# Optimization experiments

Hardware: AMD Instinct MI355X
Metric: run time of the kernel (lower is better)

## Reference

```python
import jax, jax.numpy as jnp
import numpy as np

N_NODES = 8192
N_EDGES = 131072
BATCH = 2
HID = 256      # hidden_dim
MSG = 256      # message_dim
EDIM = 64      # edge feature dim
MLP_H = 512    # message MLP hidden width
OUT = 128      # readout dim
N_ITERS = 3


def setup_inputs() -> dict:
    key = jax.random.key(0)
    ks = jax.random.split(key, 20)
    s = 0.05  # small init so iterated GRU stays well-conditioned
    inp = {
        "edge_feat": jax.random.normal(ks[0], (N_EDGES, BATCH, EDIM), jnp.float32),
        "W1": jax.random.normal(ks[1], (HID + HID + EDIM, MLP_H), jnp.float32) * s,
        "b1": jnp.zeros((MLP_H,), jnp.float32),
        "W2": jax.random.normal(ks[2], (MLP_H, MSG), jnp.float32) * s,
        "b2": jnp.zeros((MSG,), jnp.float32),
        "Wr": jax.random.normal(ks[3], (MSG, HID), jnp.float32) * s,
        "Ur": jax.random.normal(ks[4], (HID, HID), jnp.float32) * s,
        "br": jnp.zeros((HID,), jnp.float32),
        "Wz": jax.random.normal(ks[5], (MSG, HID), jnp.float32) * s,
        "Uz": jax.random.normal(ks[6], (HID, HID), jnp.float32) * s,
        "bz": jnp.zeros((HID,), jnp.float32),
        "Wh": jax.random.normal(ks[7], (MSG, HID), jnp.float32) * s,
        "Uh": jax.random.normal(ks[8], (HID, HID), jnp.float32) * s,
        "bh": jnp.zeros((HID,), jnp.float32),
        "Wo": jax.random.normal(ks[9], (HID, OUT), jnp.float32) * s,
        "bo": jnp.zeros((OUT,), jnp.float32),
        "edge_src": jax.random.randint(ks[10], (N_EDGES,), 0, N_NODES, jnp.int32),
        "edge_dst": jax.random.randint(ks[11], (N_EDGES,), 0, N_NODES, jnp.int32),
    }
    return inp


def reference(edge_feat, W1, b1, W2, b2, Wr, Ur, br, Wz, Uz, bz,
              Wh, Uh, bh, Wo, bo, edge_src, edge_dst):
    # reset_hidden_states: zeros for hidden and persistent message accumulator
    h = jnp.zeros((N_NODES, BATCH, HID), edge_feat.dtype)
    m = jnp.zeros((N_NODES, BATCH, MSG), edge_feat.dtype)

    for _ in range(N_ITERS):
        # gather endpoint hiddens: h_v = receiver (dst), h_w = sender (src)
        h_v = h[edge_dst]                       # [E, B, HID]
        h_w = h[edge_src]                       # [E, B, HID]
        x = jnp.concatenate([h_v, h_w, edge_feat], axis=-1)  # [E, B, 576]
        # per-edge message MLP
        msg = jax.nn.relu(x @ W1 + b1) @ W2 + b2              # [E, B, MSG]
        # scatter-sum into receiving nodes; accumulator persists across iters
        m = m + jax.ops.segment_sum(msg, edge_dst, num_segments=N_NODES)
        # GRU vertex update: h = GRU(m, h)
        r = jax.nn.sigmoid(m @ Wr + h @ Ur + br)
        z = jax.nn.sigmoid(m @ Wz + h @ Uz + bz)
        h_tilde = jnp.tanh(m @ Wh + (r * h) @ Uh + bh)
        h = (1.0 - z) * h + z * h_tilde

    # readout: sum node hiddens, then linear
    g = jnp.sum(h, axis=0)                      # [B, HID]
    return g @ Wo + bo                          # [B, OUT]
```

## Files before the change

kernel.cpp:

```cpp
#include <hip/hip_runtime.h>
#include <hip/hip_bf16.h>

#define E_EDGES 131072
#define NNODES  8192
#define NB      16384
#define HID     256
#define EDIM    64
#define MLPH    512
#define OUTD    128
#define NIT     3
#define RB      32

typedef short s16x4 __attribute__((ext_vector_type(4)));
typedef short s16x8 __attribute__((ext_vector_type(8)));
typedef float f32x4 __attribute__((ext_vector_type(4)));
typedef float f32x2 __attribute__((ext_vector_type(2)));

__device__ __forceinline__ short f2bf(float f){
  unsigned int x = __builtin_bit_cast(unsigned int, f);
  x += 0x7fffu + ((x >> 16) & 1u);
  return (short)(x >> 16);
}
__device__ __forceinline__ float bf2f(short s){
  unsigned int x = ((unsigned int)(unsigned short)s) << 16;
  return __builtin_bit_cast(float, x);
}
__device__ __forceinline__ void gload_lds16(const void* g, void* l){
  __builtin_amdgcn_global_load_lds(
      (const __attribute__((address_space(1))) void*)g,
      (__attribute__((address_space(3))) void*)l, 16, 0, 0);
}
#define MFMA16(a,b,c) __builtin_amdgcn_mfma_f32_16x16x32_bf16((a),(b),(c),0,0,0)

#if defined(__has_builtin)
#if __has_builtin(__builtin_amdgcn_cvt_pk_f32_fp8) && __has_builtin(__builtin_amdgcn_cvt_pk_fp8_f32)
#define FP8_HW 1
#endif
#endif
#ifndef FP8_HW
#define FP8_HW 0
#endif

__device__ __forceinline__ unsigned char enc_fp8_sw(float f){
  unsigned int b = __builtin_bit_cast(unsigned int, f);
  unsigned int s = (b >> 24) & 0x80u;
  float a = fabsf(f);
  if (a >= 448.f) return (unsigned char)(s | 0x7e);
  if (a < 0.015625f){
    int q = (int)rintf(a * 512.f);
    return (unsigned char)(s | (unsigned int)q);
  }
  unsigned int e32  = (b >> 23) & 0xff;
  unsigned int mant = b & 0x7fffff;
  unsigned int rnd  = mant + 0x7ffff + ((mant >> 20) & 1);
  unsigned int e8   = e32 - 120 + (rnd >> 23);
  unsigned int m3   = (rnd >> 20) & 7;
  if (e8 >= 16) return (unsigned char)(s | 0x7e);
  return (unsigned char)(s | (e8 << 3) | m3);
}
__device__ __forceinline__ float dec_fp8_sw(unsigned int v){
  unsigned int s = (v >> 7) & 1, e = (v >> 3) & 15, m = v & 7;
  float r;
  if (e == 0) r = (float)m * 0.001953125f;
  else        r = __builtin_bit_cast(float, ((e + 120u) << 23) | (m << 20));
  return s ? -r : r;
}
__device__ __forceinline__ unsigned char enc_fp8(float f){
#if FP8_HW
  unsigned int pk = (unsigned int)__builtin_amdgcn_cvt_pk_fp8_f32(f, f, 0, false);
  return (unsigned char)(pk & 0xff);
#else
  return enc_fp8_sw(f);
#endif
}
__device__ __forceinline__ void dec_fp8x4(unsigned int ev, float& e0, float& e1,
                                          float& e2, float& e3){
#if FP8_HW
  f32x2 lo = __builtin_amdgcn_cvt_pk_f32_fp8((int)ev, false);
  f32x2 hi = __builtin_amdgcn_cvt_pk_f32_fp8((int)ev, true);
  e0 = lo[0]; e1 = lo[1]; e2 = hi[0]; e3 = hi[1];
#else
  e0 = dec_fp8_sw(ev & 0xff); e1 = dec_fp8_sw((ev >> 8) & 0xff);
  e2 = dec_fp8_sw((ev >> 16) & 0xff); e3 = dec_fp8_sw(ev >> 24);
#endif
}

__global__ __launch_bounds__(256, 4)
void e1_gemm(const float* __restrict__ ef, const short* __restrict__ BtE,
             unsigned char* __restrict__ E1, const float* __restrict__ b1,
             const int* __restrict__ ceid)
{
  __shared__ __align__(16) short As[128 * 64];
  __shared__ __align__(16) short Bs[128 * 64];

  const int t  = threadIdx.x;
  const int w  = t >> 6, l = t & 63;
  const int lr = l & 15, lg = l >> 4;
  const int wr = w >> 1, wc = w & 1;
  const int browbase = blockIdx.x * 128;
  const int bcolbase = blockIdx.y * 128;
  const int srow = t >> 3;
  const int scol = (t & 7) * 8;

#pragma unroll
  for (int i = 0; i < 4; ++i)
    gload_lds16(BtE + (size_t)(bcolbase + srow + i * 32) * 64 + scol,
                (char*)Bs + w * 1024 + i * 4096);

#pragma unroll
  for (int i = 0; i < 4; ++i){
    int R = browbase + srow + i * 32;
    int e = ceid[R >> 1];
    const float* ap = ef + ((size_t)e * 2 + (R & 1)) * EDIM + scol;
    f32x4 f0 = *(const f32x4*)ap;
    f32x4 f1 = *(const f32x4*)(ap + 4);
    s16x8 o;
    o[0]=f2bf(f0[0]); o[1]=f2bf(f0[1]); o[2]=f2bf(f0[2]); o[3]=f2bf(f0[3]);
    o[4]=f2bf(f1[0]); o[5]=f2bf(f1[1]); o[6]=f2bf(f1[2]); o[7]=f2bf(f1[3]);
    int row = srow + i * 32;
    *(s16x8*)(As + row * 64 + (scol ^ ((row & 7) << 3))) = o;
  }
  __syncthreads();

  f32x4 acc[4][4];
#pragma unroll
  for (int mm = 0; mm < 4; ++mm)
#pragma unroll
    for (int n = 0; n < 4; ++n) acc[mm][n] = (f32x4){0.f,0.f,0.f,0.f};

#pragma unroll
  for (int kk = 0; kk < 2; ++kk){
    s16x8 a[4], b[4];
#pragma unroll
    for (int mm = 0; mm < 4; ++mm){
      int ar = wr*64 + mm*16 + lr;
      a[mm] = *(const s16x8*)(As + ar * 64 + ((kk*32 + lg*8) ^ ((ar & 7) << 3)));
    }
#pragma unroll
    for (int n = 0; n < 4; ++n){
      int br = wc*64 + n*16 + lr;
      b[n] = *(const s16x8*)(Bs + br * 64 + ((kk*32 + lg*8) ^ ((br & 7) << 3)));
    }
#pragma unroll
    for (int mm = 0; mm < 4; ++mm)
#pragma unroll
      for (int n = 0; n < 4; ++n)
        acc[mm][n] = MFMA16(a[mm], b[n], acc[mm][n]);
  }
#pragma unroll
  for (int mm = 0; mm < 4; ++mm){
    int orow0 = browbase + wr*64 + mm*16 + lg*4;
#pragma unroll
    for (int n = 0; n < 4; ++n){
      int ocol = bcolbase + wc*64 + n*16 + lr;
#pragma unroll
      for (int r = 0; r < 4; ++r)
        E1[(size_t)(orow0 + r) * MLPH + ocol] = enc_fp8(acc[mm][n][r] + b1[ocol]);
    }
  }
}

template<bool USE_P>
__global__ __launch_bounds__(256)
void edge_kernel(const short* __restrict__ P, const unsigned char* __restrict__ E1,
                 const int* __restrict__ csr_src, const int* __restrict__ row_start,
                 short* __restrict__ S)
{
  const int n = blockIdx.x;
  const int t = threadIdx.x;
  const int b = t >> 7;
  const int j = (t & 127) << 2;
  const int ps = row_start[n], pe = row_start[n + 1];

  float p10 = 0.f, p11 = 0.f, p12 = 0.f, p13 = 0.f;
  if (USE_P){
    s16x4 t1 = *(const s16x4*)(P + (size_t)(n * 2 + b) * 1024 + j);
    p10 = bf2f(t1[0]); p11 = bf2f(t1[1]); p12 = bf2f(t1[2]); p13 = bf2f(t1[3]);
  }
  float a0 = 0.f, a1 = 0.f, a2 = 0.f, a3 = 0.f;
  for (int p = ps; p < pe; ++p){
    unsigned int ev = *(const unsigned int*)(E1 + ((size_t)p * 2 + b) * 512 + j);
    float e0, e1, e2, e3;
    dec_fp8x4(ev, e0, e1, e2, e3);
    float x0 = p10 + e0, x1 = p11 + e1, x2 = p12 + e2, x3 = p13 + e3;
    if (USE_P){
      int src = csr_src[p];
      s16x4 v2 = *(const s16x4*)(P + (size_t)(src * 2 + b) * 1024 + 512 + j);
      x0 += bf2f(v2[0]); x1 += bf2f(v2[1]); x2 += bf2f(v2[2]); x3 += bf2f(v2[3]);
    }
    a0 += fmaxf(x0, 0.f); a1 += fmaxf(x1, 0.f);
    a2 += fmaxf(x2, 0.f); a3 += fmaxf(x3, 0.f);
  }
  s16x4 o; o[0] = f2bf(a0); o[1] = f2bf(a1); o[2] = f2bf(a2); o[3] = f2bf(a3);
  *(s16x4*)(S + (size_t)(n * 2 + b) * 512 + j) = o;
}

template<int PH>
__global__ __launch_bounds__(256, 2)
void node_update(const short* __restrict__ S, short* __restrict__ Pout,
                 float* __restrict__ m, float* __restrict__ h,
                 float* __restrict__ g,
                 const short* __restrict__ BtW2, const short* __restrict__ BtRZ,
                 const short* __restrict__ BtHW, const short* __restrict__ BtP,
                 const int* __restrict__ deg, const float* __restrict__ b2,
                 const float* __restrict__ br, const float* __restrict__ bz,
                 const float* __restrict__ bh)
{
  __shared__ __align__(16) char lds[69632];
  short* As = (short*)lds;
  short* Bs = (short*)(lds + 4096);
  short* Ms = (short*)(lds + 36864);
  short* Xs = (short*)(lds + 53248);
  float* Hf = (float*)lds;

  const int tid = threadIdx.x;
  const int w = tid >> 6, l = tid & 63;
  const int lr = l & 15, lg = l >> 4;
  const int grow0 = blockIdx.x * RB;

  auto stageB = [&](const short* Bt, int K, int pcol0, int k0){
#pragma unroll
    for (int i = 0; i < 8; ++i){
      int u = i * 256 + tid;
      int row = u >> 3, uc = u & 7;
      const short* gp = Bt + (size_t)(pcol0 + row) * K + k0 + ((uc ^ (row & 7)) << 3);
      gload_lds16(gp, (char*)Bs + i * 4096 + w * 1024);
    }
  };
  auto stageA_S = [&](int k0){
    int row = tid >> 3, uc = tid & 7;
    const short* gp = S + (size_t)(grow0 + row) * 512 + k0 + ((uc ^ (row & 7)) << 3);
    gload_lds16(gp, (char*)As + w * 1024);
  };
  auto rdA64 = [&](int row, int colel){ return row * 64 + (colel ^ ((row & 7) << 3)); };
  auto rd256 = [&](int row, int colel){ return row * 256 + (colel ^ ((row & 7) << 3)); };

  f32x4 hv[2][4], acc[2][4];
#pragma unroll
  for (int i = 0; i < 2; ++i)
#pragma unroll
    for (int j = 0; j < 4; ++j)
#pragma unroll
      for (int r = 0; r < 4; ++r){
        int rl = i*16 + lg*4 + r, colp = w*64 + j*16 + lr;
        size_t gi = (size_t)(grow0 + rl) * 256 + colp;
        float base = (float)deg[(grow0 + rl) >> 1] * b2[colp];
        if (PH > 0){ base += m[gi]; hv[i][j][r] = h[gi]; }
        else hv[i][j][r] = 0.f;
        acc[i][j][r] = base;
      }
  if (PH > 0){
#pragma unroll
    for (int i = 0; i < 2; ++i)
#pragma unroll
      for (int j = 0; j < 4; ++j)
#pragma unroll
        for (int r = 0; r < 4; ++r){
          int rl = i*16 + lg*4 + r, colp = w*64 + j*16 + lr;
          Xs[rd256(rl, colp)] = f2bf(hv[i][j][r]);
        }
  }

  for (int c = 0; c < 8; ++c){
    __syncthreads();
    stageA_S(c * 64);
    stageB(BtW2, 512, 0, c * 64);
    __syncthreads();
#pragma unroll
    for (int kk = 0; kk < 2; ++kk){
      s16x8 a0 = *(const s16x8*)(As + rdA64(lr,      kk*32 + lg*8));
      s16x8 a1 = *(const s16x8*)(As + rdA64(16 + lr, kk*32 + lg*8));
#pragma unroll
      for (int j = 0; j < 4; ++j){
        s16x8 bb = *(const s16x8*)(Bs + rdA64(w*64 + j*16 + lr, kk*32 + lg*8));
        acc[0][j] = MFMA16(a0, bb, acc[0][j]);
        acc[1][j] = MFMA16(a1, bb, acc[1][j]);
      }
    }
  }
#pragma unroll
  for (int i = 0; i < 2; ++i)
#pragma unroll
    for (int j = 0; j < 4; ++j)
#pragma unroll
      for (int r = 0; r < 4; ++r){
        int rl = i*16 + lg*4 + r, colp = w*64 + j*16 + lr;
        float v = acc[i][j][r];
        if (PH < 2) m[(size_t)(grow0 + rl) * 256 + colp] = v;
        Ms[rd256(rl, colp)] = f2bf(v);
      }

  const int NC = (PH > 0) ? 8 : 4;

  f32x4 Gr[2][4], Gz[2][4];
#pragma unroll
  for (int i = 0; i < 2; ++i)
#pragma unroll
    for (int j = 0; j < 4; ++j){ Gr[i][j] = (f32x4){0.f,0.f,0.f,0.f}; Gz[i][j] = (f32x4){0.f,0.f,0.f,0.f}; }

  for (int c = 0; c < NC; ++c){
    __syncthreads();
    stageB(BtRZ, 512, 0, c * 64);
    __syncthreads();
    const short* Ab = (c < 4) ? Ms : Xs;
    int kb = (c & 3) * 64;
#pragma unroll
    for (int kk = 0; kk < 2; ++kk){
      s16x8 a0 = *(const s16x8*)(Ab + rd256(lr,      kb + kk*32 + lg*8));
      s16x8 a1 = *(const s16x8*)(Ab + rd256(16 + lr, kb + kk*32 + lg*8));
#pragma unroll
      for (int j = 0; j < 4; ++j){
        s16x8 bb = *(const s16x8*)(Bs + rdA64(w*64 + j*16 + lr, kk*32 + lg*8));
        Gr[0][j] = MFMA16(a0, bb, Gr[0][j]);
        Gr[1][j] = MFMA16(a1, bb, Gr[1][j]);
      }
    }
  }
  for (int c = 0; c < NC; ++c){
    __syncthreads();
    stageB(BtRZ, 512, 256, c * 64);
    __syncthreads();
    const short* Ab = (c < 4) ? Ms : Xs;
    int kb = (c & 3) * 64;
#pragma unroll
    for (int kk = 0; kk < 2; ++kk){
      s16x8 a0 = *(const s16x8*)(Ab + rd256(lr,      kb + kk*32 + lg*8));
      s16x8 a1 = *(const s16x8*)(Ab + rd256(16 + lr, kb + kk*32 + lg*8));
#pragma unroll
      for (int j = 0; j < 4; ++j){
        s16x8 bb = *(const s16x8*)(Bs + rdA64(w*64 + j*16 + lr, kk*32 + lg*8));
        Gz[0][j] = MFMA16(a0, bb, Gz[0][j]);
        Gz[1][j] = MFMA16(a1, bb, Gz[1][j]);
      }
    }
  }

  f32x4 zz[2][4];
#pragma unroll
  for (int i = 0; i < 2; ++i)
#pragma unroll
    for (int j = 0; j < 4; ++j)
#pragma unroll
      for (int r = 0; r < 4; ++r){
        int colp = w*64 + j*16 + lr;
        zz[i][j][r] = 1.f / (1.f + __expf(-(Gz[i][j][r] + bz[colp])));
      }
  if (PH > 0){
    __syncthreads();
#pragma unroll
    for (int i = 0; i < 2; ++i)
#pragma unroll
      for (int j = 0; j < 4; ++j)
#pragma unroll
        for (int r = 0; r < 4; ++r){
          int rl = i*16 + lg*4 + r, colp = w*64 + j*16 + lr;
          float rr = 1.f / (1.f + __expf(-(Gr[i][j][r] + br[colp])));
          Xs[rd256(rl, colp)] = f2bf(rr * hv[i][j][r]);
        }
    __syncthreads();
  }

  f32x4 Gw[2][4];
#pragma unroll
  for (int i = 0; i < 2; ++i)
#pragma unroll
    for (int j = 0; j < 4; ++j) Gw[i][j] = (f32x4){0.f,0.f,0.f,0.f};
  for (int c = 0; c < NC; ++c){
    __syncthreads();
    stageB(BtHW, 512, 0, c * 64);
    __syncthreads();
    const short* Ab = (c < 4) ? Ms : Xs;
    int kb = (c & 3) * 64;
#pragma unroll
    for (int kk = 0; kk < 2; ++kk){
      s16x8 a0 = *(const s16x8*)(Ab + rd256(lr,      kb + kk*32 + lg*8));
      s16x8 a1 = *(const s16x8*)(Ab + rd256(16 + lr, kb + kk*32 + lg*8));
#pragma unroll
      for (int j = 0; j < 4; ++j){
        s16x8 bb = *(const s16x8*)(Bs + rdA64(w*64 + j*16 + lr, kk*32 + lg*8));
        Gw[0][j] = MFMA16(a0, bb, Gw[0][j]);
        Gw[1][j] = MFMA16(a1, bb, Gw[1][j]);
      }
    }
  }

  __syncthreads();
#pragma unroll
  for (int i = 0; i < 2; ++i)
#pragma unroll
    for (int j = 0; j < 4; ++j)
#pragma unroll
      for (int r = 0; r < 4; ++r){
        int rl = i*16 + lg*4 + r, colp = w*64 + j*16 + lr;
        float ht = tanhf(Gw[i][j][r] + bh[colp]);
        float z  = zz[i][j][r];
        float hn = (1.f - z) * hv[i][j][r] + z * ht;
        if (PH < 2){
          h[(size_t)(grow0 + rl) * 256 + colp] = hn;
          Ms[rd256(rl, colp)] = f2bf(hn);
        } else {
          Hf[rl * 256 + colp] = hn;
        }
      }
  __syncthreads();

  if (PH < 2){
    for (int pn = 0; pn < 4; ++pn){
      f32x4 pa0[4], pa1[4];
#pragma unroll
      for (int j = 0; j < 4; ++j){ pa0[j] = (f32x4){0.f,0.f,0.f,0.f}; pa1[j] = (f32x4){0.f,0.f,0.f,0.f}; }
      for (int c = 0; c < 4; ++c){
        __syncthreads();
        stageB(BtP, 256, pn * 256, c * 64);
        __syncthreads();
#pragma unroll
        for (int kk = 0; kk < 2; ++kk){
          s16x8 a0 = *(const s16x8*)(Ms + rd256(lr,      c*64 + kk*32 + lg*8));
          s16x8 a1 = *(const s16x8*)(Ms + rd256(16 + lr, c*64 + kk*32 + lg*8));
#pragma unroll
          for (int j = 0; j < 4; ++j){
            s16x8 bb = *(const s16x8*)(Bs + rdA64(w*64 + j*16 + lr, kk*32 + lg*8));
            pa0[j] = MFMA16(a0, bb, pa0[j]);
            pa1[j] = MFMA16(a1, bb, pa1[j]);
          }
        }
      }
#pragma unroll
      for (int j = 0; j < 4; ++j)
#pragma unroll
        for (int r = 0; r < 4; ++r){
          int colp = w*64 + j*16 + lr;
          Pout[(size_t)(grow0 + lg*4 + r)      * 1024 + pn*256 + colp] = f2bf(pa0[j][r]);
          Pout[(size_t)(grow0 + 16 + lg*4 + r) * 1024 + pn*256 + colp] = f2bf(pa1[j][r]);
        }
    }
  } else {
    float s0 = 0.f, s1 = 0.f;
#pragma unroll
    for (int rl = 0; rl < 32; rl += 2){
      s0 += Hf[rl * 256 + tid];
      s1 += Hf[(rl + 1) * 256 + tid];
    }
    atomicAdd(&g[tid], s0);
    atomicAdd(&g[256 + tid], s1);
  }
}

__global__ void count_kernel(const int* __restrict__ edst, int* __restrict__ counts){
  int e = blockIdx.x * 256 + threadIdx.x;
  if (e < E_EDGES) atomicAdd(&counts[edst[e]], 1);
}
__global__ void scan_kernel(const int* __restrict__ counts, int* __restrict__ row_start,
                            int* __restrict__ cursor){
  __shared__ int sums[1024];
  int t = threadIdx.x;
  int base = t * 8;
  int loc[8]; int s = 0;
#pragma unroll
  for (int i = 0; i < 8; ++i){ loc[i] = s; s += counts[base + i]; }
  sums[t] = s;
  __syncthreads();
  for (int o = 1; o < 1024; o <<= 1){
    int v = sums[t];
    int u = (t >= o) ? sums[t - o] : 0;
    __syncthreads();
    sums[t] = v + u;
    __syncthreads();
  }
  int excl = (t == 0) ? 0 : sums[t - 1];
#pragma unroll
  for (int i = 0; i < 8; ++i){ int v = excl + loc[i]; row_start[base + i] = v; cursor[base + i] = v; }
  if (t == 1023) row_start[NNODES] = sums[1023];
}
__global__ void fill_kernel(const int* __restrict__ edst, const int* __restrict__ esrc,
                            int* __restrict__ cursor, int* __restrict__ csr_eid,
                            int* __restrict__ csr_src){
  int e = blockIdx.x * 256 + threadIdx.x;
  if (e < E_EDGES){
    int pos = atomicAdd(&cursor[edst[e]], 1);
    csr_eid[pos] = e;
    csr_src[pos] = esrc[e];
  }
}

__global__ void prep_weights(const float* __restrict__ W1, const float* __restrict__ W2,
                             const float* __restrict__ Wr, const float* __restrict__ Ur,
                             const float* __restrict__ Wz, const float* __restrict__ Uz,
                             const float* __restrict__ Wh, const float* __restrict__ Uh,
                             short* __restrict__ BtP, short* __restrict__ BtE,
                             short* __restrict__ BtW2, short* __restrict__ BtRZ,
                             short* __restrict__ BtHW)
{
  int id = blockIdx.x * 256 + threadIdx.x;
  if (id < 262144){
    int jj = id >> 8, k = id & 255;
    float v = (jj < 512) ? W1[(size_t)k * 512 + jj] : W1[(size_t)(256 + k) * 512 + (jj - 512)];
    BtP[id] = f2bf(v);
  } else if (id < 294912){
    int i2 = id - 262144; int jj = i2 >> 6, c = i2 & 63;
    BtE[jj * 64 + (c ^ ((jj & 7) << 3))] = f2bf(W1[(size_t)(512 + c) * 512 + jj]);
  } else if (id < 425984){
    int i2 = id - 294912; int n = i2 >> 9, k = i2 & 511;
    BtW2[i2] = f2bf(W2[(size_t)k * 256 + n]);
  } else if (id < 688128){
    int i2 = id - 425984; int col = i2 >> 9, k = i2 & 511;
    float v;
    if (col < 256) v = (k < 256) ? Wr[(size_t)k * 256 + col] : Ur[(size_t)(k - 256) * 256 + col];
    else { int c2 = col - 256; v = (k < 256) ? Wz[(size_t)k * 256 + c2] : Uz[(size_t)(k - 256) * 256 + c2]; }
    BtRZ[i2] = f2bf(v);
  } else if (id < 819200){
    int i2 = id - 688128; int col = i2 >> 9, k = i2 & 511;
    float v = (k < 256) ? Wh[(size_t)k * 256 + col] : Uh[(size_t)(k - 256) * 256 + col];
    BtHW[i2] = f2bf(v);
  }
}

__global__ __launch_bounds__(256)
void readout2(const float* __restrict__ g, const float* __restrict__ Wo,
              const float* __restrict__ bo, float* __restrict__ out){
  int t = threadIdx.x;
  int b = t >> 7, o = t & 127;
  float s = bo[o];
  for (int c = 0; c < 256; ++c) s += g[b * 256 + c] * Wo[c * 128 + o];
  out[b * 128 + o] = s;
}

extern "C" void kernel_launch(void* const* d_in, const int* in_sizes, int n_in,
                              void* d_out, int out_size, void* d_ws, size_t ws_size,
                              hipStream_t stream)
{
  const float* ef  = (const float*)d_in[0];
  const float* W1  = (const float*)d_in[1];
  const float* b1  = (const float*)d_in[2];
  const float* W2  = (const float*)d_in[3];
  const float* b2  = (const float*)d_in[4];
  const float* Wr  = (const float*)d_in[5];
  const float* Ur  = (const float*)d_in[6];
  const float* br  = (const float*)d_in[7];
  const float* Wz  = (const float*)d_in[8];
  const float* Uz  = (const float*)d_in[9];
  const float* bz  = (const float*)d_in[10];
  const float* Wh  = (const float*)d_in[11];
  const float* Uh  = (const float*)d_in[12];
  const float* bh  = (const float*)d_in[13];
  const float* Wo  = (const float*)d_in[14];
  const float* bo  = (const float*)d_in[15];
  const int* esrc  = (const int*)d_in[16];
  const int* edst  = (const int*)d_in[17];

  char* base = (char*)d_ws;
  size_t off = 0;
  auto alloc = [&](size_t bytes) -> char* {
    off = (off + 255) & ~(size_t)255;
    char* p = base + off;
    off += bytes;
    return p;
  };
  float* h    = (float*)alloc((size_t)NB * 256 * 4);
  float* m    = (float*)alloc((size_t)NB * 256 * 4);
  short* P    = (short*)alloc((size_t)NB * 1024 * 2);
  short* S    = (short*)alloc((size_t)NB * 512 * 2);
  unsigned char* E1 = (unsigned char*)alloc((size_t)E_EDGES * 2 * MLPH);
  short* BtP  = (short*)alloc(262144 * 2);
  short* BtE  = (short*)alloc(32768 * 2);
  short* BtW2 = (short*)alloc(131072 * 2);
  short* BtRZ = (short*)alloc(262144 * 2);
  short* BtHW = (short*)alloc(131072 * 2);
  int* counts = (int*)alloc(NNODES * 4);
  int* rs     = (int*)alloc((NNODES + 1) * 4);
  int* cursor = (int*)alloc(NNODES * 4);
  int* ceid   = (int*)alloc(E_EDGES * 4);
  int* csrc   = (int*)alloc(E_EDGES * 4);
  float* g    = (float*)alloc(512 * 4);

  dim3 blk(256);

  hipMemsetAsync(g,  0, 512 * 4, stream);
  hipMemsetAsync(counts, 0, NNODES * 4, stream);
  prep_weights<<<3200, blk, 0, stream>>>(W1, W2, Wr, Ur, Wz, Uz, Wh, Uh,
                                         BtP, BtE, BtW2, BtRZ, BtHW);
  count_kernel<<<512, blk, 0, stream>>>(edst, counts);
  scan_kernel<<<1, 1024, 0, stream>>>(counts, rs, cursor);
  fill_kernel<<<512, blk, 0, stream>>>(edst, esrc, cursor, ceid, csrc);

  e1_gemm<<<dim3(E_EDGES * 2 / 128, MLPH / 128), blk, 0, stream>>>(
      ef, BtE, E1, b1, ceid);

  edge_kernel<false><<<NNODES, blk, 0, stream>>>(P, E1, csrc, rs, S);
  node_update<0><<<NB / RB, blk, 0, stream>>>(S, P, m, h, g,
      BtW2, BtRZ, BtHW, BtP, counts, b2, br, bz, bh);

  edge_kernel<true><<<NNODES, blk, 0, stream>>>(P, E1, csrc, rs, S);
  node_update<1><<<NB / RB, blk, 0, stream>>>(S, P, m, h, g,
      BtW2, BtRZ, BtHW, BtP, counts, b2, br, bz, bh);

  edge_kernel<true><<<NNODES, blk, 0, stream>>>(P, E1, csrc, rs, S);
  node_update<2><<<NB / RB, blk, 0, stream>>>(S, P, m, h, g,
      BtW2, BtRZ, BtHW, BtP, counts, b2, br, bz, bh);

  readout2<<<1, blk, 0, stream>>>(g, Wo, bo, (float*)d_out);
}
```

Measured before the change: 455.4 us.

## Split node_update across 8 waves and swap e1_gemm MFMA operands for packed stores

node_update now launches 512 threads (8 waves) per 32-row block. Each wave owns 16 rows by 64 columns instead of 32 by 64, which halves the accumulator registers per thread and the B-staging loads per thread, aiming for more waves in flight to hide latency. Separately, e1_gemm swaps its MFMA operands so that each lane holds 4 consecutive output columns. That allows one packed 32-bit fp8 store per lane and a vectorized bias load, replacing scattered byte stores. The trade-off in node_update is that each B-fragment load from LDS now feeds only one MFMA instead of two, so LDS read traffic per MFMA roughly doubles.

```diff
diff --git a/kernel.cpp b/kernel.cpp
--- a/kernel.cpp
+++ b/kernel.cpp
@@ -124,38 +124,41 @@
 
   f32x4 acc[4][4];
 #pragma unroll
-  for (int mm = 0; mm < 4; ++mm)
-#pragma unroll
-    for (int n = 0; n < 4; ++n) acc[mm][n] = (f32x4){0.f,0.f,0.f,0.f};
+  for (int mf = 0; mf < 4; ++mf)
+#pragma unroll
+    for (int e2 = 0; e2 < 4; ++e2) acc[mf][e2] = (f32x4){0.f,0.f,0.f,0.f};
 
 #pragma unroll
   for (int kk = 0; kk < 2; ++kk){
     s16x8 a[4], b[4];
 #pragma unroll
-    for (int mm = 0; mm < 4; ++mm){
-      int ar = wr*64 + mm*16 + lr;
-      a[mm] = *(const s16x8*)(As + ar * 64 + ((kk*32 + lg*8) ^ ((ar & 7) << 3)));
-    }
-#pragma unroll
-    for (int n = 0; n < 4; ++n){
-      int br = wc*64 + n*16 + lr;
-      b[n] = *(const s16x8*)(Bs + br * 64 + ((kk*32 + lg*8) ^ ((br & 7) << 3)));
-    }
-#pragma unroll
-    for (int mm = 0; mm < 4; ++mm)
-#pragma unroll
-      for (int n = 0; n < 4; ++n)
-        acc[mm][n] = MFMA16(a[mm], b[n], acc[mm][n]);
-  }
-#pragma unroll
-  for (int mm = 0; mm < 4; ++mm){
-    int orow0 = browbase + wr*64 + mm*16 + lg*4;
-#pragma unroll
-    for (int n = 0; n < 4; ++n){
-      int ocol = bcolbase + wc*64 + n*16 + lr;
-#pragma unroll
-      for (int r = 0; r < 4; ++r)
-        E1[(size_t)(orow0 + r) * MLPH + ocol] = enc_fp8(acc[mm][n][r] + b1[ocol]);
+    for (int e2 = 0; e2 < 4; ++e2){
+      int ar = wr*64 + e2*16 + lr;
+      a[e2] = *(const s16x8*)(As + ar * 64 + ((kk*32 + lg*8) ^ ((ar & 7) << 3)));
+    }
+#pragma unroll
+    for (int mf = 0; mf < 4; ++mf){
+      int br = wc*64 + mf*16 + lr;
+      b[mf] = *(const s16x8*)(Bs + br * 64 + ((kk*32 + lg*8) ^ ((br & 7) << 3)));
+    }
+#pragma unroll
+    for (int mf = 0; mf < 4; ++mf)
+#pragma unroll
+      for (int e2 = 0; e2 < 4; ++e2)
+        acc[mf][e2] = MFMA16(b[mf], a[e2], acc[mf][e2]);
+  }
+#pragma unroll
+  for (int mf = 0; mf < 4; ++mf){
+    int mcol0 = bcolbase + wc*64 + mf*16 + lg*4;
+    f32x4 bv = *(const f32x4*)(b1 + mcol0);
+#pragma unroll
+    for (int e2 = 0; e2 < 4; ++e2){
+      int erow = browbase + wr*64 + e2*16 + lr;
+      unsigned int pk = (unsigned int)enc_fp8(acc[mf][e2][0] + bv[0])
+                      | ((unsigned int)enc_fp8(acc[mf][e2][1] + bv[1]) << 8)
+                      | ((unsigned int)enc_fp8(acc[mf][e2][2] + bv[2]) << 16)
+                      | ((unsigned int)enc_fp8(acc[mf][e2][3] + bv[3]) << 24);
+      *(unsigned int*)(E1 + (size_t)erow * MLPH + mcol0) = pk;
     }
   }
 }
@@ -196,7 +199,7 @@
 }
 
 template<int PH>
-__global__ __launch_bounds__(256, 2)
+__global__ __launch_bounds__(512, 4)
 void node_update(const short* __restrict__ S, short* __restrict__ Pout,
                  float* __restrict__ m, float* __restrict__ h,
                  float* __restrict__ g,
@@ -216,49 +219,49 @@
   const int tid = threadIdx.x;
   const int w = tid >> 6, l = tid & 63;
   const int lr = l & 15, lg = l >> 4;
+  const int wq = w >> 2, wc = w & 3;
   const int grow0 = blockIdx.x * RB;
 
   auto stageB = [&](const short* Bt, int K, int pcol0, int k0){
 #pragma unroll
-    for (int i = 0; i < 8; ++i){
-      int u = i * 256 + tid;
+    for (int i = 0; i < 4; ++i){
+      int u = i * 512 + tid;
       int row = u >> 3, uc = u & 7;
       const short* gp = Bt + (size_t)(pcol0 + row) * K + k0 + ((uc ^ (row & 7)) << 3);
-      gload_lds16(gp, (char*)Bs + i * 4096 + w * 1024);
+      gload_lds16(gp, (char*)Bs + i * 8192 + w * 1024);
     }
   };
   auto stageA_S = [&](int k0){
-    int row = tid >> 3, uc = tid & 7;
-    const short* gp = S + (size_t)(grow0 + row) * 512 + k0 + ((uc ^ (row & 7)) << 3);
-    gload_lds16(gp, (char*)As + w * 1024);
+    if (w < 4){
+      int u = w * 64 + l;
+      int row = u >> 3, uc = u & 7;
+      const short* gp = S + (size_t)(grow0 + row) * 512 + k0 + ((uc ^ (row & 7)) << 3);
+      gload_lds16(gp, (char*)As + w * 1024);
+    }
   };
   auto rdA64 = [&](int row, int colel){ return row * 64 + (colel ^ ((row & 7) << 3)); };
   auto rd256 = [&](int row, int colel){ return row * 256 + (colel ^ ((row & 7) << 3)); };
 
-  f32x4 hv[2][4], acc[2][4];
-#pragma unroll
-  for (int i = 0; i < 2; ++i)
+  f32x4 hv[4], acc[4];
+#pragma unroll
+  for (int j = 0; j < 4; ++j)
+#pragma unroll
+    for (int r = 0; r < 4; ++r){
+      int rl = wq*16 + lg*4 + r, colp = wc*64 + j*16 + lr;
+      size_t gi = (size_t)(grow0 + rl) * 256 + colp;
+      float base = (float)deg[(grow0 + rl) >> 1] * b2[colp];
+      if (PH > 0){ base += m[gi]; hv[j][r] = h[gi]; }
+      else hv[j][r] = 0.f;
+      acc[j][r] = base;
+    }
+  if (PH > 0){
 #pragma unroll
     for (int j = 0; j < 4; ++j)
 #pragma unroll
       for (int r = 0; r < 4; ++r){
-        int rl = i*16 + lg*4 + r, colp = w*64 + j*16 + lr;
-        size_t gi = (size_t)(grow0 + rl) * 256 + colp;
-        float base = (float)deg[(grow0 + rl) >> 1] * b2[colp];
-        if (PH > 0){ base += m[gi]; hv[i][j][r] = h[gi]; }
-        else hv[i][j][r] = 0.f;
-        acc[i][j][r] = base;
-      }
-  if (PH > 0){
-#pragma unroll
-    for (int i = 0; i < 2; ++i)
-#pragma unroll
-      for (int j = 0; j < 4; ++j)
-#pragma unroll
-        for (int r = 0; r < 4; ++r){
-          int rl = i*16 + lg*4 + r, colp = w*64 + j*16 + lr;
-          Xs[rd256(rl, colp)] = f2bf(hv[i][j][r]);
-        }
+        int rl = wq*16 + lg*4 + r, colp = wc*64 + j*16 + lr;
+        Xs[rd256(rl, colp)] = f2bf(hv[j][r]);
+      }
   }
 
   for (int c = 0; c < 8; ++c){
@@ -268,35 +271,29 @@
     __syncthreads();
 #pragma unroll
     for (int kk = 0; kk < 2; ++kk){
-      s16x8 a0 = *(const s16x8*)(As + rdA64(lr,      kk*32 + lg*8));
-      s16x8 a1 = *(const s16x8*)(As + rdA64(16 + lr, kk*32 + lg*8));
+      s16x8 a0 = *(const s16x8*)(As + rdA64(wq*16 + lr, kk*32 + lg*8));
 #pragma unroll
       for (int j = 0; j < 4; ++j){
-        s16x8 bb = *(const s16x8*)(Bs + rdA64(w*64 + j*16 + lr, kk*32 + lg*8));
-        acc[0][j] = MFMA16(a0, bb, acc[0][j]);
-        acc[1][j] = MFMA16(a1, bb, acc[1][j]);
-      }
-    }
-  }
-#pragma unroll
-  for (int i = 0; i < 2; ++i)
-#pragma unroll
-    for (int j = 0; j < 4; ++j)
-#pragma unroll
-      for (int r = 0; r < 4; ++r){
-        int rl = i*16 + lg*4 + r, colp = w*64 + j*16 + lr;
-        float v = acc[i][j][r];
-        if (PH < 2) m[(size_t)(grow0 + rl) * 256 + colp] = v;
-        Ms[rd256(rl, colp)] = f2bf(v);
-      }
+        s16x8 bb = *(const s16x8*)(Bs + rdA64(wc*64 + j*16 + lr, kk*32 + lg*8));
+        acc[j] = MFMA16(a0, bb, acc[j]);
+      }
+    }
+  }
+#pragma unroll
+  for (int j = 0; j < 4; ++j)
+#pragma unroll
+    for (int r = 0; r < 4; ++r){
+      int rl = wq*16 + lg*4 + r, colp = wc*64 + j*16 + lr;
+      float v = acc[j][r];
+      if (PH < 2) m[(size_t)(grow0 + rl) * 256 + colp] = v;
+      Ms[rd256(rl, colp)] = f2bf(v);
+    }
 
   const int NC = (PH > 0) ? 8 : 4;
 
-  f32x4 Gr[2][4], Gz[2][4];
-#pragma unroll
-  for (int i = 0; i < 2; ++i)
-#pragma unroll
-    for (int j = 0; j < 4; ++j){ Gr[i][j] = (f32x4){0.f,0.f,0.f,0.f}; Gz[i][j] = (f32x4){0.f,0.f,0.f,0.f}; }
+  f32x4 Gr[4], Gz[4];
+#pragma unroll
+  for (int j = 0; j < 4; ++j){ Gr[j] = (f32x4){0.f,0.f,0.f,0.f}; Gz[j] = (f32x4){0.f,0.f,0.f,0.f}; }
 
   for (int c = 0; c < NC; ++c){
     __syncthreads();
@@ -306,13 +303,11 @@
     int kb = (c & 3) * 64;
 #pragma unroll
     for (int kk = 0; kk < 2; ++kk){
-      s16x8 a0 = *(const s16x8*)(Ab + rd256(lr,      kb + kk*32 + lg*8));
-      s16x8 a1 = *(const s16x8*)(Ab + rd256(16 + lr, kb + kk*32 + lg*8));
+      s16x8 a0 = *(const s16x8*)(Ab + rd256(wq*16 + lr, kb + kk*32 + lg*8));
 #pragma unroll
       for (int j = 0; j < 4; ++j){
-        s16x8 bb = *(const s16x8*)(Bs + rdA64(w*64 + j*16 + lr, kk*32 + lg*8));
-        Gr[0][j] = MFMA16(a0, bb, Gr[0][j]);
-        Gr[1][j] = MFMA16(a1, bb, Gr[1][j]);
+        s16x8 bb = *(const s16x8*)(Bs + rdA64(wc*64 + j*16 + lr, kk*32 + lg*8));
+        Gr[j] = MFMA16(a0, bb, Gr[j]);
       }
     }
   }
@@ -324,47 +319,39 @@
     int kb = (c & 3) * 64;
 #pragma unroll
     for (int kk = 0; kk < 2; ++kk){
-      s16x8 a0 = *(const s16x8*)(Ab + rd256(lr,      kb + kk*32 + lg*8));
-      s16x8 a1 = *(const s16x8*)(Ab + rd256(16 + lr, kb + kk*32 + lg*8));
+      s16x8 a0 = *(const s16x8*)(Ab + rd256(wq*16 + lr, kb + kk*32 + lg*8));
 #pragma unroll
       for (int j = 0; j < 4; ++j){
-        s16x8 bb = *(const s16x8*)(Bs + rdA64(w*64 + j*16 + lr, kk*32 + lg*8));
-        Gz[0][j] = MFMA16(a0, bb, Gz[0][j]);
-        Gz[1][j] = MFMA16(a1, bb, Gz[1][j]);
-      }
-    }
-  }
-
-  f32x4 zz[2][4];
-#pragma unroll
-  for (int i = 0; i < 2; ++i)
+        s16x8 bb = *(const s16x8*)(Bs + rdA64(wc*64 + j*16 + lr, kk*32 + lg*8));
+        Gz[j] = MFMA16(a0, bb, Gz[j]);
+      }
+    }
+  }
+
+  f32x4 zz[4];
+#pragma unroll
+  for (int j = 0; j < 4; ++j)
+#pragma unroll
+    for (int r = 0; r < 4; ++r){
+      int colp = wc*64 + j*16 + lr;
+      zz[j][r] = 1.f / (1.f + __expf(-(Gz[j][r] + bz[colp])));
+    }
+  if (PH > 0){
+    __syncthreads();
 #pragma unroll
     for (int j = 0; j < 4; ++j)
 #pragma unroll
       for (int r = 0; r < 4; ++r){
-        int colp = w*64 + j*16 + lr;
-        zz[i][j][r] = 1.f / (1.f + __expf(-(Gz[i][j][r] + bz[colp])));
-      }
-  if (PH > 0){
-    __syncthreads();
-#pragma unroll
-    for (int i = 0; i < 2; ++i)
-#pragma unroll
-      for (int j = 0; j < 4; ++j)
-#pragma unroll
-        for (int r = 0; r < 4; ++r){
-          int rl = i*16 + lg*4 + r, colp = w*64 + j*16 + lr;
-          float rr = 1.f / (1.f + __expf(-(Gr[i][j][r] + br[colp])));
-          Xs[rd256(rl, colp)] = f2bf(rr * hv[i][j][r]);
-        }
-    __syncthreads();
-  }
-
-  f32x4 Gw[2][4];
-#pragma unroll
-  for (int i = 0; i < 2; ++i)
-#pragma unroll
-    for (int j = 0; j < 4; ++j) Gw[i][j] = (f32x4){0.f,0.f,0.f,0.f};
+        int rl = wq*16 + lg*4 + r, colp = wc*64 + j*16 + lr;
+        float rr = 1.f / (1.f + __expf(-(Gr[j][r] + br[colp])));
+        Xs[rd256(rl, colp)] = f2bf(rr * hv[j][r]);
+      }
+    __syncthreads();
+  }
+
+  f32x4 Gw[4];
+#pragma unroll
+  for (int j = 0; j < 4; ++j) Gw[j] = (f32x4){0.f,0.f,0.f,0.f};
   for (int c = 0; c < NC; ++c){
     __syncthreads();
     stageB(BtHW, 512, 0, c * 64);
@@ -373,55 +360,49 @@
     int kb = (c & 3) * 64;
 #pragma unroll
     for (int kk = 0; kk < 2; ++kk){
-      s16x8 a0 = *(const s16x8*)(Ab + rd256(lr,      kb + kk*32 + lg*8));
-      s16x8 a1 = *(const s16x8*)(Ab + rd256(16 + lr, kb + kk*32 + lg*8));
+      s16x8 a0 = *(const s16x8*)(Ab + rd256(wq*16 + lr, kb + kk*32 + lg*8));
 #pragma unroll
       for (int j = 0; j < 4; ++j){
-        s16x8 bb = *(const s16x8*)(Bs + rdA64(w*64 + j*16 + lr, kk*32 + lg*8));
-        Gw[0][j] = MFMA16(a0, bb, Gw[0][j]);
-        Gw[1][j] = MFMA16(a1, bb, Gw[1][j]);
+        s16x8 bb = *(const s16x8*)(Bs + rdA64(wc*64 + j*16 + lr, kk*32 + lg*8));
+        Gw[j] = MFMA16(a0, bb, Gw[j]);
       }
     }
   }
 
   __syncthreads();
 #pragma unroll
-  for (int i = 0; i < 2; ++i)
-#pragma unroll
-    for (int j = 0; j < 4; ++j)
-#pragma unroll
-      for (int r = 0; r < 4; ++r){
-        int rl = i*16 + lg*4 + r, colp = w*64 + j*16 + lr;
-        float ht = tanhf(Gw[i][j][r] + bh[colp]);
-        float z  = zz[i][j][r];
-        float hn = (1.f - z) * hv[i][j][r] + z * ht;
-        if (PH < 2){
-          h[(size_t)(grow0 + rl) * 256 + colp] = hn;
-          Ms[rd256(rl, colp)] = f2bf(hn);
-        } else {
-          Hf[rl * 256 + colp] = hn;
-        }
-      }
+  for (int j = 0; j < 4; ++j)
+#pragma unroll
+    for (int r = 0; r < 4; ++r){
+      int rl = wq*16 + lg*4 + r, colp = wc*64 + j*16 + lr;
+      float ht = tanhf(Gw[j][r] + bh[colp]);
+      float z  = zz[j][r];
+      float hn = (1.f - z) * hv[j][r] + z * ht;
+      if (PH < 2){
+        h[(size_t)(grow0 + rl) * 256 + colp] = hn;
+        Ms[rd256(rl, colp)] = f2bf(hn);
+      } else {
+        Hf[rl * 256 + colp] = hn;
+      }
+    }
   __syncthreads();
 
   if (PH < 2){
     for (int pn = 0; pn < 4; ++pn){
-      f32x4 pa0[4], pa1[4];
-#pragma unroll
-      for (int j = 0; j < 4; ++j){ pa0[j] = (f32x4){0.f,0.f,0.f,0.f}; pa1[j] = (f32x4){0.f,0.f,0.f,0.f}; }
+      f32x4 pa[4];
+#pragma unroll
+      for (int j = 0; j < 4; ++j) pa[j] = (f32x4){0.f,0.f,0.f,0.f};
       for (int c = 0; c < 4; ++c){
         __syncthreads();
         stageB(BtP, 256, pn * 256, c * 64);
         __syncthreads();
 #pragma unroll
         for (int kk = 0; kk < 2; ++kk){
-          s16x8 a0 = *(const s16x8*)(Ms + rd256(lr,      c*64 + kk*32 + lg*8));
-          s16x8 a1 = *(const s16x8*)(Ms + rd256(16 + lr, c*64 + kk*32 + lg*8));
+          s16x8 a0 = *(const s16x8*)(Ms + rd256(wq*16 + lr, c*64 + kk*32 + lg*8));
 #pragma unroll
           for (int j = 0; j < 4; ++j){
-            s16x8 bb = *(const s16x8*)(Bs + rdA64(w*64 + j*16 + lr, kk*32 + lg*8));
-            pa0[j] = MFMA16(a0, bb, pa0[j]);
-            pa1[j] = MFMA16(a1, bb, pa1[j]);
+            s16x8 bb = *(const s16x8*)(Bs + rdA64(wc*64 + j*16 + lr, kk*32 + lg*8));
+            pa[j] = MFMA16(a0, bb, pa[j]);
           }
         }
       }
@@ -429,20 +410,17 @@
       for (int j = 0; j < 4; ++j)
 #pragma unroll
         for (int r = 0; r < 4; ++r){
-          int colp = w*64 + j*16 + lr;
-          Pout[(size_t)(grow0 + lg*4 + r)      * 1024 + pn*256 + colp] = f2bf(pa0[j][r]);
-          Pout[(size_t)(grow0 + 16 + lg*4 + r) * 1024 + pn*256 + colp] = f2bf(pa1[j][r]);
+          int colp = wc*64 + j*16 + lr;
+          Pout[(size_t)(grow0 + wq*16 + lg*4 + r) * 1024 + pn*256 + colp] = f2bf(pa[j][r]);
         }
     }
   } else {
-    float s0 = 0.f, s1 = 0.f;
-#pragma unroll
-    for (int rl = 0; rl < 32; rl += 2){
-      s0 += Hf[rl * 256 + tid];
-      s1 += Hf[(rl + 1) * 256 + tid];
-    }
-    atomicAdd(&g[tid], s0);
-    atomicAdd(&g[256 + tid], s1);
+    int col = tid & 255, pb = (tid >> 8) & 1;
+    float s = 0.f;
+#pragma unroll
+    for (int rr = 0; rr < 16; ++rr)
+      s += Hf[(2*rr + pb) * 256 + col];
+    atomicAdd(&g[pb * 256 + col], s);
   }
 }
 
@@ -587,15 +565,15 @@
       ef, BtE, E1, b1, ceid);
 
   edge_kernel<false><<<NNODES, blk, 0, stream>>>(P, E1, csrc, rs, S);
-  node_update<0><<<NB / RB, blk, 0, stream>>>(S, P, m, h, g,
+  node_update<0><<<NB / RB, dim3(512), 0, stream>>>(S, P, m, h, g,
       BtW2, BtRZ, BtHW, BtP, counts, b2, br, bz, bh);
 
   edge_kernel<true><<<NNODES, blk, 0, stream>>>(P, E1, csrc, rs, S);
-  node_update<1><<<NB / RB, blk, 0, stream>>>(S, P, m, h, g,
+  node_update<1><<<NB / RB, dim3(512), 0, stream>>>(S, P, m, h, g,
       BtW2, BtRZ, BtHW, BtP, counts, b2, br, bz, bh);
 
   edge_kernel<true><<<NNODES, blk, 0, stream>>>(P, E1, csrc, rs, S);
-  node_update<2><<<NB / RB, blk, 0, stream>>>(S, P, m, h, g,
+  node_update<2><<<NB / RB, dim3(512), 0, stream>>>(S, P, m, h, g,
       BtW2, BtRZ, BtHW, BtP, counts, b2, br, bz, bh);
 
   readout2<<<1, blk, 0, stream>>>(g, Wo, bo, (float*)d_out);
```

Measured after the change: 461.3 us. About the same (+1.3%).
